# Kernel optimization log

Hardware: AMD Instinct MI355X
Metric: run time of the kernel (lower is better)

Reference implementation:

```python
import math
import jax, jax.numpy as jnp
import numpy as np

E = 1024
H = 16
D = E // H  # head_dim = 64
B, T = 4, 2048


def setup_inputs() -> dict:
    key = jax.random.key(0)
    ks = jax.random.split(key, 9)
    s = 1.0 / math.sqrt(E)
    inp = {
        "x": jax.random.normal(ks[0], (B, T, E), dtype=jnp.float32),
        "Wq": jax.random.uniform(ks[1], (E, E), jnp.float32, -s, s),
        "bq": jax.random.uniform(ks[2], (E,), jnp.float32, -s, s),
        "Wk": jax.random.uniform(ks[3], (E, E), jnp.float32, -s, s),
        "bk": jax.random.uniform(ks[4], (E,), jnp.float32, -s, s),
        "Wv": jax.random.uniform(ks[5], (E, E), jnp.float32, -s, s),
        "bv": jax.random.uniform(ks[6], (E,), jnp.float32, -s, s),
        "Wo": jax.random.uniform(ks[7], (E, E), jnp.float32, -s, s),
        "bo": jax.random.uniform(ks[8], (E,), jnp.float32, -s, s),
    }
    return inp


def reference(x, Wq, bq, Wk, bk, Wv, bv, Wo, bo):
    # Linear projections (torch Linear: y = x @ W.T + b)
    q = x @ Wq.T + bq
    k = x @ Wk.T + bk
    v = x @ Wv.T + bv
    # [B, T, E] -> [B, H, T, D]
    def split_heads(t):
        return t.reshape(B, T, H, D).transpose(0, 2, 1, 3)
    q, k, v = split_heads(q), split_heads(k), split_heads(v)
    # scaled dot-product attention; note scale uses head_dim (attention(self.head_dim))
    scores = jnp.einsum("bhqd,bhkd->bhqk", q, k) / math.sqrt(D)
    attn = jax.nn.softmax(scores, axis=-1)
    out = jnp.einsum("bhqk,bhkd->bhqd", attn, v)
    out = out.transpose(0, 2, 1, 3).reshape(B, T, E)
    return out @ Wo.T + bo
```

## Files before the change

kernel.cpp:

```cpp
#include <hip/hip_runtime.h>

typedef short bh8 __attribute__((ext_vector_type(8)));
typedef short bh4 __attribute__((ext_vector_type(4)));
typedef float f4 __attribute__((ext_vector_type(4)));
typedef unsigned int u32;
typedef u32 u32x2 __attribute__((ext_vector_type(2)));
typedef u32 u32x4 __attribute__((ext_vector_type(4)));

#if __has_builtin(__builtin_amdgcn_exp2f)
#define EXP2(x) __builtin_amdgcn_exp2f(x)
#else
#define EXP2(x) exp2f(x)
#endif

__device__ __forceinline__ short f2bf(float f) {
  unsigned u = __float_as_uint(f);
  u += 0x7FFFu + ((u >> 16) & 1u);
  return (short)(u >> 16);
}

__device__ __forceinline__ void async16(const void* g, void* l) {
  __builtin_amdgcn_global_load_lds((const __attribute__((address_space(1))) void*)g,
                                   (__attribute__((address_space(3))) void*)l, 16, 0, 0);
}

__global__ void cvt_all(const float* __restrict__ x, const float* __restrict__ Wq,
                        const float* __restrict__ Wk, const float* __restrict__ Wv,
                        const float* __restrict__ Wo, short* __restrict__ xb,
                        short* __restrict__ wqb) {
  int i = blockIdx.x * blockDim.x + threadIdx.x;
  const float* src;
  short* dst;
  int idx;
  if (i < (1 << 21)) {
    src = x; dst = xb; idx = i;
  } else {
    int j = i - (1 << 21);
    int w = j >> 18;
    idx = j & ((1 << 18) - 1);
    src = w == 0 ? Wq : w == 1 ? Wk : w == 2 ? Wv : Wo;
    dst = wqb + ((size_t)w << 20);
  }
  f4 v = *(const f4*)(src + (size_t)idx * 4);
  bh4 o;
  o[0] = f2bf(v[0]); o[1] = f2bf(v[1]); o[2] = f2bf(v[2]); o[3] = f2bf(v[3]);
  *(bh4*)(dst + (size_t)idx * 4) = o;
}

template <typename OutT, bool BROW>
__device__ __forceinline__ void gemm_body(const short* __restrict__ A, const short* __restrict__ Bw,
                                          const float* __restrict__ bias, OutT* __restrict__ C,
                                          int m0, int n0, int N, int K, float scale,
                                          short* a_lds, short* b_lds) {
  const int t = threadIdx.x;
  const int lane = t & 63, wave = t >> 6, quad = lane >> 4, l15 = lane & 15;
  const int mw = (wave >> 1) * 64, nw = (wave & 1) * 64;

  f4 acc[4][4];
#pragma unroll
  for (int i = 0; i < 4; ++i)
#pragma unroll
    for (int j = 0; j < 4; ++j) acc[i][j] = (f4){0.f, 0.f, 0.f, 0.f};

  for (int k0 = 0; k0 < K; k0 += 64) {
    __syncthreads();
#pragma unroll
    for (int i = 0; i < 4; ++i) {
      int c = i * 256 + t;
      int m = c >> 3;
      int kq = (c & 7) ^ (m & 7);
      async16(A + (size_t)(m0 + m) * K + k0 + kq * 8, (char*)a_lds + c * 16);
    }
#pragma unroll
    for (int i = 0; i < 4; ++i) {
      int c = i * 256 + t;
      int m = c >> 3;
      int kq = (c & 7) ^ (m & 7);
      async16(Bw + (size_t)(n0 + m) * K + k0 + kq * 8, (char*)b_lds + c * 16);
    }
    __syncthreads();

#pragma unroll
    for (int s = 0; s < 2; ++s) {
      bh8 af[4], bfr[4];
#pragma unroll
      for (int ms = 0; ms < 4; ++ms) {
        int m = mw + ms * 16 + l15;
        int pos = m * 8 + ((s * 4 + quad) ^ (m & 7));
        af[ms] = *(const bh8*)(a_lds + pos * 8);
      }
#pragma unroll
      for (int ns = 0; ns < 4; ++ns) {
        int n = nw + ns * 16 + l15;
        int pos = n * 8 + ((s * 4 + quad) ^ (n & 7));
        bfr[ns] = *(const bh8*)(b_lds + pos * 8);
      }
#pragma unroll
      for (int ms = 0; ms < 4; ++ms)
#pragma unroll
        for (int ns = 0; ns < 4; ++ns)
          acc[ms][ns] = __builtin_amdgcn_mfma_f32_16x16x32_bf16(af[ms], bfr[ns], acc[ms][ns], 0, 0, 0);
    }
  }
#pragma unroll
  for (int ns = 0; ns < 4; ++ns) {
    int col = n0 + nw + ns * 16 + l15;
    float bcol = BROW ? 0.f : bias[col & 1023];
#pragma unroll
    for (int ms = 0; ms < 4; ++ms) {
      int row = m0 + mw + ms * 16 + quad * 4;
#pragma unroll
      for (int r = 0; r < 4; ++r) {
        float bv = BROW ? bias[(row + r) & 1023] : bcol;
        float v = (acc[ms][ns][r] + bv) * scale;
        if (sizeof(OutT) == 2)
          ((short*)C)[(size_t)(row + r) * N + col] = f2bf(v);
        else
          ((float*)C)[(size_t)(row + r) * N + col] = v;
      }
    }
  }
}

__global__ void gemm_qkv(const short* __restrict__ xb, const short* __restrict__ W3,
                         const float* __restrict__ bq, const float* __restrict__ bk,
                         const float* __restrict__ bv,
                         short* __restrict__ Qo, short* __restrict__ Ko, short* __restrict__ VTo,
                         float qscale) {
  __shared__ __align__(16) short a_lds[128 * 64];
  __shared__ __align__(16) short b_lds[128 * 64];
  const int linear = blockIdx.y * 24 + blockIdx.x;
  const int xcd = linear & 7;
  const int slot = linear >> 3;
  const int byp = xcd * 8 + slot / 24;
  const int rest = slot % 24;
  const int which = rest >> 3;
  const int nx = rest & 7;
  if (which == 2) {
    const short* Wv = W3 + (size_t)2 * 1024 * 1024;
    gemm_body<short, true>(Wv, xb, bv, VTo, nx * 128, byp * 128,
                           8192, 1024, 1.0f, a_lds, b_lds);
  } else {
    const short* Bw = W3 + (size_t)which * 1024 * 1024;
    const float* bias = which == 0 ? bq : bk;
    short* C = which == 0 ? Qo : Ko;
    float scale = which == 0 ? qscale : 1.0f;
    gemm_body<short, false>(xb, Bw, bias, C, byp * 128, nx * 128,
                            1024, 1024, scale, a_lds, b_lds);
  }
}

__global__ void gemm_bt_f32(const short* __restrict__ A, const short* __restrict__ Bw,
                            const float* __restrict__ bias, float* __restrict__ C) {
  __shared__ __align__(16) short a_lds[128 * 64];
  __shared__ __align__(16) short b_lds[128 * 64];
  const int linear = blockIdx.y * 8 + blockIdx.x;
  const int xcd = linear & 7;
  const int slot = linear >> 3;
  const int byp = xcd * 8 + (slot >> 3);
  const int bxp = slot & 7;
  gemm_body<float, false>(A, Bw, bias, C, byp * 128, bxp * 128, 1024, 1024, 1.0f,
                          a_lds, b_lds);
}

__global__ void attn_kernel(const short* __restrict__ Qb, const short* __restrict__ Kb,
                            const short* __restrict__ VTb, short* __restrict__ AO) {
  __shared__ __align__(16) short k_lds[64 * 64];
  __shared__ __align__(16) short vt_lds[64 * 64];
  const int t = threadIdx.x, lane = t & 63, wave = t >> 6, quad = lane >> 4, l15 = lane & 15;
  const int linear = blockIdx.y * 16 + blockIdx.x;
  const int xcd = linear & 7;
  const int slot = linear >> 3;
  const int bh = xcd * 8 + (slot >> 4);
  const int qx = slot & 15;
  const int b = bh >> 4, h = bh & 15;
  const int q0 = qx * 128;
  const size_t baseq = ((size_t)b * 2048) * 1024 + (size_t)h * 64;
  const size_t basev = ((size_t)h * 64) * 8192 + (size_t)b * 2048;

  bh8 qf[2][2];
#pragma unroll
  for (int mi = 0; mi < 2; ++mi)
#pragma unroll
    for (int ks = 0; ks < 2; ++ks)
      qf[mi][ks] = *(const bh8*)(Qb + baseq + (size_t)(q0 + wave * 32 + mi * 16 + l15) * 1024 + ks * 32 + quad * 8);

  f4 O[2][4];
  float l_part[2] = {0.f, 0.f};
#pragma unroll
  for (int mi = 0; mi < 2; ++mi)
#pragma unroll
    for (int di = 0; di < 4; ++di) O[mi][di] = (f4){0.f, 0.f, 0.f, 0.f};

  for (int kt = 0; kt < 2048; kt += 64) {
    __syncthreads();
#pragma unroll
    for (int i = 0; i < 2; ++i) {
      int c = i * 256 + t;
      int kk = c >> 3;
      int dq = (c & 7) ^ (kk & 7);
      async16(Kb + baseq + (size_t)(kt + kk) * 1024 + dq * 8,
              (char*)k_lds + (i * 256 + wave * 64) * 16);
    }
#pragma unroll
    for (int i = 0; i < 2; ++i) {
      int c = i * 256 + t;
      int d = c >> 3;
      int kc = (c & 7) ^ (d & 7);
      async16(VTb + basev + (size_t)d * 8192 + kt + kc * 8,
              (char*)vt_lds + (i * 256 + wave * 64) * 16);
    }
    __syncthreads();

    f4 ST[4][2];
#pragma unroll
    for (int mK = 0; mK < 4; ++mK) {
      int key = mK * 16 + l15;
      bh8 ka0 = *(const bh8*)(k_lds + (key * 8 + (quad ^ (key & 7))) * 8);
      bh8 ka1 = *(const bh8*)(k_lds + (key * 8 + ((quad + 4) ^ (key & 7))) * 8);
#pragma unroll
      for (int mi = 0; mi < 2; ++mi) {
        f4 s = (f4){-16.f, -16.f, -16.f, -16.f};
        s = __builtin_amdgcn_mfma_f32_16x16x32_bf16(ka0, qf[mi][0], s, 0, 0, 0);
        s = __builtin_amdgcn_mfma_f32_16x16x32_bf16(ka1, qf[mi][1], s, 0, 0, 0);
        ST[mK][mi] = s;
      }
    }

    bh8 pa[2][2];
#pragma unroll
    for (int mi = 0; mi < 2; ++mi) {
      float lp = 0.f;
      u32 E[4], F[4];
#pragma unroll
      for (int mK = 0; mK < 4; ++mK) {
        float p0 = EXP2(ST[mK][mi][0]);
        float p1 = EXP2(ST[mK][mi][1]);
        float p2 = EXP2(ST[mK][mi][2]);
        float p3 = EXP2(ST[mK][mi][3]);
        lp += (p0 + p1) + (p2 + p3);
        E[mK] = __builtin_amdgcn_perm(__float_as_uint(p1), __float_as_uint(p0), 0x07060302u);
        F[mK] = __builtin_amdgcn_perm(__float_as_uint(p3), __float_as_uint(p2), 0x07060302u);
      }
      l_part[mi] += lp;
#pragma unroll
      for (int ks = 0; ks < 2; ++ks) {
        u32 e0 = E[ks * 2], e1 = E[ks * 2 + 1];
        u32 f0 = F[ks * 2], f1 = F[ks * 2 + 1];
        asm volatile("v_permlane32_swap_b32 %0, %1" : "+v"(e0), "+v"(e1));
        asm volatile("v_permlane16_swap_b32 %0, %1" : "+v"(e0), "+v"(e1));
        asm volatile("v_permlane32_swap_b32 %0, %1" : "+v"(f0), "+v"(f1));
        asm volatile("v_permlane16_swap_b32 %0, %1" : "+v"(f0), "+v"(f1));
        u32x4 w;
        w[0] = e0; w[1] = f0; w[2] = e1; w[3] = f1;
        pa[mi][ks] = __builtin_bit_cast(bh8, w);
      }
    }

#pragma unroll
    for (int di = 0; di < 4; ++di) {
      int d = di * 16 + l15;
      bh8 vb0 = *(const bh8*)(vt_lds + (d * 8 + (quad ^ (d & 7))) * 8);
      bh8 vb1 = *(const bh8*)(vt_lds + (d * 8 + ((quad + 4) ^ (d & 7))) * 8);
#pragma unroll
      for (int mi = 0; mi < 2; ++mi) {
        f4 o = O[mi][di];
        o = __builtin_amdgcn_mfma_f32_16x16x32_bf16(pa[mi][0], vb0, o, 0, 0, 0);
        o = __builtin_amdgcn_mfma_f32_16x16x32_bf16(pa[mi][1], vb1, o, 0, 0, 0);
        O[mi][di] = o;
      }
    }
  }

#pragma unroll
  for (int mi = 0; mi < 2; ++mi) {
    float l0 = l_part[mi];
    l0 += __shfl_xor(l0, 16);
    l0 += __shfl_xor(l0, 32);
    float rl[4];
#pragma unroll
    for (int r = 0; r < 4; ++r) {
      float lb = __shfl(l0, quad * 4 + r);
      rl[r] = __builtin_amdgcn_rcpf(lb);
    }
#pragma unroll
    for (int di = 0; di < 4; ++di)
#pragma unroll
      for (int r = 0; r < 4; ++r) {
        int row = q0 + wave * 32 + mi * 16 + quad * 4 + r;
        AO[baseq + (size_t)row * 1024 + di * 16 + l15] = f2bf(O[mi][di][r] * rl[r]);
      }
  }
}

extern "C" void kernel_launch(void* const* d_in, const int* in_sizes, int n_in,
                              void* d_out, int out_size, void* d_ws, size_t ws_size,
                              hipStream_t stream) {
  const float* x  = (const float*)d_in[0];
  const float* Wq = (const float*)d_in[1];
  const float* bq = (const float*)d_in[2];
  const float* Wk = (const float*)d_in[3];
  const float* bk = (const float*)d_in[4];
  const float* Wv = (const float*)d_in[5];
  const float* bv = (const float*)d_in[6];
  const float* Wo = (const float*)d_in[7];
  const float* bo = (const float*)d_in[8];
  float* out = (float*)d_out;

  const int M = 8192, E = 1024;
  const size_t NX = (size_t)M * E;
  const size_t NW = (size_t)E * E;

  short* ws  = (short*)d_ws;
  short* xb  = ws;
  short* wqb = xb + NX;
  short* wob = wqb + 3 * NW;
  short* qb  = wob + NW;
  short* kb  = qb + NX;
  short* vt  = kb + NX;
  short* aob = xb;

  cvt_all<<<dim3(12288), 256, 0, stream>>>(x, Wq, Wk, Wv, Wo, xb, wqb);

  const float qscale = 0.18033688011112042f;
  gemm_qkv<<<dim3(24, 64), 256, 0, stream>>>(xb, wqb, bq, bk, bv, qb, kb, vt, qscale);

  attn_kernel<<<dim3(16, 64), 256, 0, stream>>>(qb, kb, vt, aob);

  gemm_bt_f32<<<dim3(8, 64), 256, 0, stream>>>(aob, wob, bo, out);
}
```

Baseline: 266.5 us.

## Double-buffer LDS tiles in attention and output-projection GEMM

Adds a double-buffered LDS path to the GEMM body, used only by the output-projection GEMM, and to the attention kernel's K/V^T tiles. The next tile's async global-to-LDS loads are issued before the current tile's MFMA work, and there is one wait-plus-barrier per iteration instead of two syncthreads. The goal is to hide global load latency behind compute. It doubles LDS use per block, which can lower occupancy, and it relies on manual vmcnt waits and barriers for correctness.

```diff
diff --git a/kernel.cpp b/kernel.cpp
--- a/kernel.cpp
+++ b/kernel.cpp
@@ -47,7 +47,7 @@
   *(bh4*)(dst + (size_t)idx * 4) = o;
 }
 
-template <typename OutT, bool BROW>
+template <typename OutT, bool BROW, bool DBUF>
 __device__ __forceinline__ void gemm_body(const short* __restrict__ A, const short* __restrict__ Bw,
                                           const float* __restrict__ bias, OutT* __restrict__ C,
                                           int m0, int n0, int N, int K, float scale,
@@ -62,24 +62,40 @@
 #pragma unroll
     for (int j = 0; j < 4; ++j) acc[i][j] = (f4){0.f, 0.f, 0.f, 0.f};
 
-  for (int k0 = 0; k0 < K; k0 += 64) {
-    __syncthreads();
+  auto stage = [&](int k0, int buf) {
 #pragma unroll
     for (int i = 0; i < 4; ++i) {
       int c = i * 256 + t;
       int m = c >> 3;
       int kq = (c & 7) ^ (m & 7);
-      async16(A + (size_t)(m0 + m) * K + k0 + kq * 8, (char*)a_lds + c * 16);
+      async16(A + (size_t)(m0 + m) * K + k0 + kq * 8, (char*)(a_lds + buf * 8192) + c * 16);
     }
 #pragma unroll
     for (int i = 0; i < 4; ++i) {
       int c = i * 256 + t;
       int m = c >> 3;
       int kq = (c & 7) ^ (m & 7);
-      async16(Bw + (size_t)(n0 + m) * K + k0 + kq * 8, (char*)b_lds + c * 16);
-    }
-    __syncthreads();
-
+      async16(Bw + (size_t)(n0 + m) * K + k0 + kq * 8, (char*)(b_lds + buf * 8192) + c * 16);
+    }
+  };
+
+  int cur = 0;
+  if constexpr (DBUF) {
+    stage(0, 0);
+    asm volatile("s_waitcnt vmcnt(0)" ::: "memory");
+    __builtin_amdgcn_s_barrier();
+    asm volatile("" ::: "memory");
+  }
+  for (int k0 = 0; k0 < K; k0 += 64) {
+    if constexpr (DBUF) {
+      if (k0 + 64 < K) stage(k0 + 64, cur ^ 1);
+    } else {
+      __syncthreads();
+      stage(k0, 0);
+      __syncthreads();
+    }
+    const short* al = a_lds + cur * 8192;
+    const short* bl = b_lds + cur * 8192;
 #pragma unroll
     for (int s = 0; s < 2; ++s) {
       bh8 af[4], bfr[4];
@@ -87,19 +103,25 @@
       for (int ms = 0; ms < 4; ++ms) {
         int m = mw + ms * 16 + l15;
         int pos = m * 8 + ((s * 4 + quad) ^ (m & 7));
-        af[ms] = *(const bh8*)(a_lds + pos * 8);
+        af[ms] = *(const bh8*)(al + pos * 8);
       }
 #pragma unroll
       for (int ns = 0; ns < 4; ++ns) {
         int n = nw + ns * 16 + l15;
         int pos = n * 8 + ((s * 4 + quad) ^ (n & 7));
-        bfr[ns] = *(const bh8*)(b_lds + pos * 8);
+        bfr[ns] = *(const bh8*)(bl + pos * 8);
       }
 #pragma unroll
       for (int ms = 0; ms < 4; ++ms)
 #pragma unroll
         for (int ns = 0; ns < 4; ++ns)
           acc[ms][ns] = __builtin_amdgcn_mfma_f32_16x16x32_bf16(af[ms], bfr[ns], acc[ms][ns], 0, 0, 0);
+    }
+    if constexpr (DBUF) {
+      asm volatile("s_waitcnt vmcnt(0)" ::: "memory");
+      __builtin_amdgcn_s_barrier();
+      asm volatile("" ::: "memory");
+      cur ^= 1;
     }
   }
 #pragma unroll
@@ -138,35 +160,35 @@
   const int nx = rest & 7;
   if (which == 2) {
     const short* Wv = W3 + (size_t)2 * 1024 * 1024;
-    gemm_body<short, true>(Wv, xb, bv, VTo, nx * 128, byp * 128,
-                           8192, 1024, 1.0f, a_lds, b_lds);
+    gemm_body<short, true, false>(Wv, xb, bv, VTo, nx * 128, byp * 128,
+                                  8192, 1024, 1.0f, a_lds, b_lds);
   } else {
     const short* Bw = W3 + (size_t)which * 1024 * 1024;
     const float* bias = which == 0 ? bq : bk;
     short* C = which == 0 ? Qo : Ko;
     float scale = which == 0 ? qscale : 1.0f;
-    gemm_body<short, false>(xb, Bw, bias, C, byp * 128, nx * 128,
-                            1024, 1024, scale, a_lds, b_lds);
+    gemm_body<short, false, false>(xb, Bw, bias, C, byp * 128, nx * 128,
+                                   1024, 1024, scale, a_lds, b_lds);
   }
 }
 
 __global__ void gemm_bt_f32(const short* __restrict__ A, const short* __restrict__ Bw,
                             const float* __restrict__ bias, float* __restrict__ C) {
-  __shared__ __align__(16) short a_lds[128 * 64];
-  __shared__ __align__(16) short b_lds[128 * 64];
+  __shared__ __align__(16) short a_lds[2 * 128 * 64];
+  __shared__ __align__(16) short b_lds[2 * 128 * 64];
   const int linear = blockIdx.y * 8 + blockIdx.x;
   const int xcd = linear & 7;
   const int slot = linear >> 3;
   const int byp = xcd * 8 + (slot >> 3);
   const int bxp = slot & 7;
-  gemm_body<float, false>(A, Bw, bias, C, byp * 128, bxp * 128, 1024, 1024, 1.0f,
-                          a_lds, b_lds);
+  gemm_body<float, false, true>(A, Bw, bias, C, byp * 128, bxp * 128, 1024, 1024, 1.0f,
+                                a_lds, b_lds);
 }
 
 __global__ void attn_kernel(const short* __restrict__ Qb, const short* __restrict__ Kb,
                             const short* __restrict__ VTb, short* __restrict__ AO) {
-  __shared__ __align__(16) short k_lds[64 * 64];
-  __shared__ __align__(16) short vt_lds[64 * 64];
+  __shared__ __align__(16) short k_lds[2][64 * 64];
+  __shared__ __align__(16) short vt_lds[2][64 * 64];
   const int t = threadIdx.x, lane = t & 63, wave = t >> 6, quad = lane >> 4, l15 = lane & 15;
   const int linear = blockIdx.y * 16 + blockIdx.x;
   const int xcd = linear & 7;
@@ -192,15 +214,14 @@
 #pragma unroll
     for (int di = 0; di < 4; ++di) O[mi][di] = (f4){0.f, 0.f, 0.f, 0.f};
 
-  for (int kt = 0; kt < 2048; kt += 64) {
-    __syncthreads();
+  auto stageKV = [&](int buf, int kt) {
 #pragma unroll
     for (int i = 0; i < 2; ++i) {
       int c = i * 256 + t;
       int kk = c >> 3;
       int dq = (c & 7) ^ (kk & 7);
       async16(Kb + baseq + (size_t)(kt + kk) * 1024 + dq * 8,
-              (char*)k_lds + (i * 256 + wave * 64) * 16);
+              (char*)(k_lds[buf]) + (i * 256 + wave * 64) * 16);
     }
 #pragma unroll
     for (int i = 0; i < 2; ++i) {
@@ -208,16 +229,27 @@
       int d = c >> 3;
       int kc = (c & 7) ^ (d & 7);
       async16(VTb + basev + (size_t)d * 8192 + kt + kc * 8,
-              (char*)vt_lds + (i * 256 + wave * 64) * 16);
-    }
-    __syncthreads();
+              (char*)(vt_lds[buf]) + (i * 256 + wave * 64) * 16);
+    }
+  };
+
+  stageKV(0, 0);
+  asm volatile("s_waitcnt vmcnt(0)" ::: "memory");
+  __builtin_amdgcn_s_barrier();
+  asm volatile("" ::: "memory");
+
+  int cur = 0;
+  for (int kt = 0; kt < 2048; kt += 64) {
+    if (kt + 64 < 2048) stageKV(cur ^ 1, kt + 64);
+    const short* kl = k_lds[cur];
+    const short* vl = vt_lds[cur];
 
     f4 ST[4][2];
 #pragma unroll
     for (int mK = 0; mK < 4; ++mK) {
       int key = mK * 16 + l15;
-      bh8 ka0 = *(const bh8*)(k_lds + (key * 8 + (quad ^ (key & 7))) * 8);
-      bh8 ka1 = *(const bh8*)(k_lds + (key * 8 + ((quad + 4) ^ (key & 7))) * 8);
+      bh8 ka0 = *(const bh8*)(kl + (key * 8 + (quad ^ (key & 7))) * 8);
+      bh8 ka1 = *(const bh8*)(kl + (key * 8 + ((quad + 4) ^ (key & 7))) * 8);
 #pragma unroll
       for (int mi = 0; mi < 2; ++mi) {
         f4 s = (f4){-16.f, -16.f, -16.f, -16.f};
@@ -260,8 +292,8 @@
 #pragma unroll
     for (int di = 0; di < 4; ++di) {
       int d = di * 16 + l15;
-      bh8 vb0 = *(const bh8*)(vt_lds + (d * 8 + (quad ^ (d & 7))) * 8);
-      bh8 vb1 = *(const bh8*)(vt_lds + (d * 8 + ((quad + 4) ^ (d & 7))) * 8);
+      bh8 vb0 = *(const bh8*)(vl + (d * 8 + (quad ^ (d & 7))) * 8);
+      bh8 vb1 = *(const bh8*)(vl + (d * 8 + ((quad + 4) ^ (d & 7))) * 8);
 #pragma unroll
       for (int mi = 0; mi < 2; ++mi) {
         f4 o = O[mi][di];
@@ -270,6 +302,11 @@
         O[mi][di] = o;
       }
     }
+
+    asm volatile("s_waitcnt vmcnt(0)" ::: "memory");
+    __builtin_amdgcn_s_barrier();
+    asm volatile("" ::: "memory");
+    cur ^= 1;
   }
 
 #pragma unroll
```

After: 303.5 us. 13.9% more time.
